# Performance work log

Measured on AMD Instinct MI355X. Metric: run time of the kernel, lower is better.

Reference implementation:

```python
import jax, jax.numpy as jnp
import numpy as np

EPS = 1e-6
ROPE_THETA = 1000000.0
SPAN_LENGTHS = [700, 300, 600, 448]
L, D, H, HK, DH, FF = 2, 2048, 16, 8, 128, 8192


def _rmsnorm(x, w):
    var = jnp.mean(jnp.square(x), axis=-1, keepdims=True)
    return x * jax.lax.rsqrt(var + EPS) * w


def _rotate_half(x):
    x1, x2 = jnp.split(x, 2, axis=-1)
    return jnp.concatenate([-x2, x1], axis=-1)


def setup_inputs() -> dict:
    key = jax.random.key(0)
    ks = jax.random.split(key, 8)
    s = 0.02  # init scale
    seg = np.repeat(np.arange(len(SPAN_LENGTHS), dtype=np.int32), SPAN_LENGTHS)
    pos = np.concatenate([np.arange(n, dtype=np.int32) for n in SPAN_LENGTHS])
    T = seg.shape[0]
    return {
        "hidden_states": jax.random.normal(ks[0], (T, D), jnp.float32),
        "ln1_w": jnp.ones((L, D), jnp.float32),
        "ln2_w": jnp.ones((L, D), jnp.float32),
        "wq": jax.random.normal(ks[1], (L, D, H * DH), jnp.float32) * s,
        "wk": jax.random.normal(ks[2], (L, D, HK * DH), jnp.float32) * s,
        "wv": jax.random.normal(ks[3], (L, D, HK * DH), jnp.float32) * s,
        "wo": jax.random.normal(ks[4], (L, H * DH, D), jnp.float32) * s,
        "qn_w": jnp.ones((L, DH), jnp.float32),
        "kn_w": jnp.ones((L, DH), jnp.float32),
        "wg": jax.random.normal(ks[5], (L, D, FF), jnp.float32) * s,
        "wu": jax.random.normal(ks[6], (L, D, FF), jnp.float32) * s,
        "wd": jax.random.normal(ks[7], (L, FF, D), jnp.float32) * s,
        "final_norm_w": jnp.ones((D,), jnp.float32),
        "segment_ids": jnp.asarray(seg),
        "position_ids": jnp.asarray(pos),
    }


def reference(hidden_states, ln1_w, ln2_w, wq, wk, wv, wo, qn_w, kn_w, wg, wu, wd, final_norm_w, segment_ids, position_ids):
    T = hidden_states.shape[0]
    # rotary tables from per-request positions (positions reset per span)
    inv_freq = 1.0 / (ROPE_THETA ** (jnp.arange(0, DH, 2, dtype=jnp.float32) / DH))
    freqs = position_ids.astype(jnp.float32)[:, None] * inv_freq  # [T, DH/2]
    emb = jnp.concatenate([freqs, freqs], axis=-1)                # [T, DH]
    cos = jnp.cos(emb)[:, None, :]
    sin = jnp.sin(emb)[:, None, :]
    # ragged causal mask: attend only within the same request span, causally
    tok = jnp.arange(T)
    mask = (segment_ids[:, None] == segment_ids[None, :]) & (tok[:, None] >= tok[None, :])
    neg = jnp.finfo(hidden_states.dtype).min
    scale = 1.0 / np.sqrt(DH)

    x = hidden_states
    for l in range(L):
        h = _rmsnorm(x, ln1_w[l])
        q = (h @ wq[l]).reshape(T, H, DH)
        k = (h @ wk[l]).reshape(T, HK, DH)
        v = (h @ wv[l]).reshape(T, HK, DH)
        q = _rmsnorm(q, qn_w[l])  # Qwen3 per-head q/k RMSNorm
        k = _rmsnorm(k, kn_w[l])
        q = q * cos + _rotate_half(q) * sin
        k = k * cos + _rotate_half(k) * sin
        rep = H // HK  # GQA
        k = jnp.repeat(k, rep, axis=1)
        v = jnp.repeat(v, rep, axis=1)
        scores = jnp.einsum('thd,shd->hts', q, k) * scale  # [H, T, T]
        scores = jnp.where(mask[None], scores, neg)
        attn = jax.nn.softmax(scores, axis=-1)
        o = jnp.einsum('hts,shd->thd', attn, v).reshape(T, H * DH)
        x = x + o @ wo[l]
        h = _rmsnorm(x, ln2_w[l])
        x = x + (jax.nn.silu(h @ wg[l]) * (h @ wu[l])) @ wd[l]
    return _rmsnorm(x, final_norm_w)
```

## Files before the change

### kernel.cpp

```cpp
#include <hip/hip_runtime.h>
#include <stdint.h>

#define T_SEQ 2048
#define DMODEL 2048
#define NH 16
#define NKV 8
#define DHEAD 128
#define DFF 8192

typedef float f32x4 __attribute__((ext_vector_type(4)));
typedef float f32x2 __attribute__((ext_vector_type(2)));
typedef __bf16 bf16x8 __attribute__((ext_vector_type(8)));
typedef unsigned short ushort8 __attribute__((ext_vector_type(8)));
typedef unsigned short ushort_t;

typedef __attribute__((address_space(1))) void gvoid;
typedef __attribute__((address_space(3))) void lvoid;

__device__ inline unsigned short f2bf(float f) {
  unsigned int u = __float_as_uint(f);
  u += 0x7fffu + ((u >> 16) & 1u);
  return (unsigned short)(u >> 16);
}
__device__ inline float bf2f(unsigned short h) {
  return __uint_as_float(((unsigned int)h) << 16);
}

__device__ inline void gload_lds16(const void* g, void* l) {
  __builtin_amdgcn_global_load_lds((gvoid*)g, (lvoid*)l, 16, 0, 0);
}

template <typename TIN>
__device__ __forceinline__ void transpose_tile(const TIN* __restrict__ in,
                                               ushort_t* __restrict__ out,
                                               int R, int C, int rmode,
                                               int bx, int by) {
  __shared__ float tile[64 * 72];
  int tid = threadIdx.x;
  int r0 = by * 64, c0 = bx * 64;
  int rl = tid >> 4;
  int cc = tid & 15;
#pragma unroll
  for (int i = 0; i < 4; ++i) {
    int row = rl + i * 16;
    const TIN* src = in + (size_t)(r0 + row) * C + c0 + cc * 4;
    float v0, v1, v2, v3;
    if constexpr (sizeof(TIN) == 4) {
      f32x4 v = *(const f32x4*)src;
      v0 = v.x; v1 = v.y; v2 = v.z; v3 = v.w;
    } else {
      ushort4 v = *(const ushort4*)src;
      v0 = bf2f(v.x); v1 = bf2f(v.y); v2 = bf2f(v.z); v3 = bf2f(v.w);
    }
    int chunk = cc ^ (row & 15);
    f32x4 t = {v0, v1, v2, v3};
    *(f32x4*)&tile[row * 72 + chunk * 4] = t;
  }
  __syncthreads();
#pragma unroll
  for (int i = 0; i < 4; ++i) {
    int nrow = rl + i * 16;
    int k4 = cc * 4;
    ushort4 o;
    {
      int k = k4 + 0;
      o.x = f2bf(tile[k * 72 + (((nrow >> 2) ^ (k & 15)) << 2) + (nrow & 3)]);
      k = k4 + 1;
      o.y = f2bf(tile[k * 72 + (((nrow >> 2) ^ (k & 15)) << 2) + (nrow & 3)]);
      k = k4 + 2;
      o.z = f2bf(tile[k * 72 + (((nrow >> 2) ^ (k & 15)) << 2) + (nrow & 3)]);
      k = k4 + 3;
      o.w = f2bf(tile[k * 72 + (((nrow >> 2) ^ (k & 15)) << 2) + (nrow & 3)]);
    }
    int n = c0 + nrow;
    int orow = n;
    if (rmode == 1) orow = ((n >> 4) << 5) + (n & 15);
    else if (rmode == 2) orow = ((n >> 4) << 5) + 16 + (n & 15);
    *(ushort4*)(out + (size_t)orow * R + r0 + k4) = o;
  }
}

template <typename TIN>
__global__ __launch_bounds__(256) void k_transpose_bf16(const TIN* __restrict__ in,
                                                        ushort_t* __restrict__ out,
                                                        int R, int C, int rmode) {
  transpose_tile<TIN>(in, out, R, C, rmode, blockIdx.x, blockIdx.y);
}

__global__ __launch_bounds__(256) void k_transpose_qkv(const float* __restrict__ wq,
                                                       const float* __restrict__ wk,
                                                       const float* __restrict__ wv,
                                                       ushort_t* __restrict__ out) {
  int z = blockIdx.z;
  const float* in;
  ushort_t* o;
  int C;
  if (z == 0) { in = wq; o = out; C = 2048; }
  else if (z == 1) { in = wk; o = out + (size_t)2048 * 2048; C = 1024; }
  else { in = wv; o = out + (size_t)3072 * 2048; C = 1024; }
  if ((int)blockIdx.x * 64 >= C) return;
  transpose_tile<float>(in, o, 2048, C, 0, blockIdx.x, blockIdx.y);
}

__global__ __launch_bounds__(256) void k_transpose_gu(const float* __restrict__ wg,
                                                      const float* __restrict__ wu,
                                                      ushort_t* __restrict__ out) {
  int z = blockIdx.z;
  transpose_tile<float>(z ? wu : wg, out, 2048, 8192, z ? 2 : 1,
                        blockIdx.x, blockIdx.y);
}

template <int BF16OUT>
__global__ __launch_bounds__(256) void k_rmsnorm(const float* __restrict__ X,
                                                 const float* __restrict__ W,
                                                 void* __restrict__ OUT) {
  int row = blockIdx.x, tid = threadIdx.x;
  const float* xr = X + (size_t)row * DMODEL;
  f32x4 x0 = *(const f32x4*)(xr + tid * 4);
  f32x4 x1 = *(const f32x4*)(xr + 1024 + tid * 4);
  float ss = x0.x * x0.x + x0.y * x0.y + x0.z * x0.z + x0.w * x0.w +
             x1.x * x1.x + x1.y * x1.y + x1.z * x1.z + x1.w * x1.w;
#pragma unroll
  for (int o = 1; o < 64; o <<= 1) ss += __shfl_xor(ss, o, 64);
  __shared__ float red[4];
  int w = tid >> 6;
  if ((tid & 63) == 0) red[w] = ss;
  __syncthreads();
  float tot = red[0] + red[1] + red[2] + red[3];
  float sc = rsqrtf(tot / (float)DMODEL + 1e-6f);
  f32x4 w0 = *(const f32x4*)(W + tid * 4);
  f32x4 w1 = *(const f32x4*)(W + 1024 + tid * 4);
  if constexpr (BF16OUT) {
    ushort_t* o = (ushort_t*)OUT + (size_t)row * DMODEL;
    ushort4 a, b;
    a.x = f2bf(x0.x * sc * w0.x); a.y = f2bf(x0.y * sc * w0.y);
    a.z = f2bf(x0.z * sc * w0.z); a.w = f2bf(x0.w * sc * w0.w);
    b.x = f2bf(x1.x * sc * w1.x); b.y = f2bf(x1.y * sc * w1.y);
    b.z = f2bf(x1.z * sc * w1.z); b.w = f2bf(x1.w * sc * w1.w);
    *(ushort4*)(o + tid * 4) = a;
    *(ushort4*)(o + 1024 + tid * 4) = b;
  } else {
    float* o = (float*)OUT + (size_t)row * DMODEL;
    f32x4 a = {x0.x * sc * w0.x, x0.y * sc * w0.y, x0.z * sc * w0.z, x0.w * sc * w0.w};
    f32x4 b = {x1.x * sc * w1.x, x1.y * sc * w1.y, x1.z * sc * w1.z, x1.w * sc * w1.w};
    *(f32x4*)(o + tid * 4) = a;
    *(f32x4*)(o + 1024 + tid * 4) = b;
  }
}

template <int NZ, int WRITEH>
__global__ __launch_bounds__(512) void k_redln(const ushort_t* __restrict__ P,
                                               const float* __restrict__ RES,
                                               const float* __restrict__ W,
                                               float* __restrict__ OUT,
                                               ushort_t* __restrict__ HB) {
  int row = blockIdx.x, tid = threadIdx.x;
  size_t base = (size_t)row * DMODEL + tid * 4;
  f32x4 v = *(const f32x4*)(RES + base);
#pragma unroll
  for (int z = 0; z < NZ; ++z) {
    ushort4 t = *(const ushort4*)(P + (size_t)z * T_SEQ * DMODEL + base);
    v.x += bf2f(t.x); v.y += bf2f(t.y); v.z += bf2f(t.z); v.w += bf2f(t.w);
  }
  if constexpr (WRITEH != 2) *(f32x4*)(OUT + base) = v;
  if constexpr (WRITEH >= 1) {
    float ss = v.x * v.x + v.y * v.y + v.z * v.z + v.w * v.w;
#pragma unroll
    for (int o = 1; o < 64; o <<= 1) ss += __shfl_xor(ss, o, 64);
    __shared__ float red[8];
    if ((tid & 63) == 0) red[tid >> 6] = ss;
    __syncthreads();
    float tot = 0.f;
#pragma unroll
    for (int i = 0; i < 8; ++i) tot += red[i];
    float sc = rsqrtf(tot / (float)DMODEL + 1e-6f);
    f32x4 wv = *(const f32x4*)(W + tid * 4);
    if constexpr (WRITEH == 1) {
      ushort4 h;
      h.x = f2bf(v.x * sc * wv.x); h.y = f2bf(v.y * sc * wv.y);
      h.z = f2bf(v.z * sc * wv.z); h.w = f2bf(v.w * sc * wv.w);
      *(ushort4*)(HB + base) = h;
    } else {
      f32x4 o = {v.x * sc * wv.x, v.y * sc * wv.y, v.z * sc * wv.z, v.w * sc * wv.w};
      *(f32x4*)(OUT + base) = o;
    }
  }
}

#define EPI_STOREB 3
#define EPI_GLU 5

#define LOADB(dst, bs, rbase)                                                  \
  {                                                                            \
    _Pragma("unroll") for (int ks = 0; ks < 2; ++ks)                           \
        _Pragma("unroll") for (int ni = 0; ni < 2; ++ni)                       \
            dst[ks][ni] = *(const bf16x8*)((bs) +                              \
                (((rbase) + ni * 16 + lr) << 6) +                              \
                ((((ks << 2) + lg) ^ (lr & 7)) << 3));                         \
  }

#define MFMA_Q(q, B)                                                           \
  {                                                                            \
    _Pragma("unroll") for (int ks = 0; ks < 2; ++ks)                           \
        _Pragma("unroll") for (int mi = 0; mi < 4; ++mi)                       \
            _Pragma("unroll") for (int ni = 0; ni < 2; ++ni)                   \
                acc[mi][(q) * 2 + ni] =                                        \
                    __builtin_amdgcn_mfma_f32_16x16x32_bf16(                   \
                        af[ks][mi], B[ks][ni], acc[mi][(q) * 2 + ni], 0, 0, 0); \
  }

template <int LAST>
__device__ __forceinline__ void g256_iter(
    const ushort_t* __restrict__ as, const ushort_t* __restrict__ bsA,
    const ushort_t* __restrict__ bsB, ushort_t* __restrict__ nA,
    ushort_t* __restrict__ nB, const ushort_t* __restrict__ an,
    const ushort_t* __restrict__ bn, size_t rs, int slds, int lr, int lg,
    f32x4 (&acc)[4][8]) {
  bf16x8 af[2][4], b0[2][2], b1[2][2];
#pragma unroll
  for (int ks = 0; ks < 2; ++ks)
#pragma unroll
    for (int mi = 0; mi < 4; ++mi)
      af[ks][mi] = *(const bf16x8*)(as + ((mi * 16 + lr) << 6) +
                                    ((((ks << 2) + lg) ^ (lr & 7)) << 3));
  LOADB(b0, bsA, 0);
  if constexpr (!LAST) {
    gload_lds16(an, nA + slds);
    gload_lds16(an + rs, nA + 4096 + slds);
    gload_lds16(an + 2 * rs, nA + 8192 + slds);
    gload_lds16(an + 3 * rs, nA + 12288 + slds);
    gload_lds16(bn, nB + slds);
    gload_lds16(bn + rs, nB + 4096 + slds);
    gload_lds16(bn + 2 * rs, nB + 8192 + slds);
    gload_lds16(bn + 3 * rs, nB + 12288 + slds);
  }
  LOADB(b1, bsA, 32);
  asm volatile("s_waitcnt lgkmcnt(4)" ::: "memory");
  __builtin_amdgcn_sched_barrier(0);
  __builtin_amdgcn_s_setprio(1);
  MFMA_Q(0, b0);
  __builtin_amdgcn_s_setprio(0);
  LOADB(b0, bsB, 0);
  asm volatile("s_waitcnt lgkmcnt(4)" ::: "memory");
  __builtin_amdgcn_sched_barrier(0);
  __builtin_amdgcn_s_setprio(1);
  MFMA_Q(1, b1);
  __builtin_amdgcn_s_setprio(0);
  LOADB(b1, bsB, 32);
  asm volatile("s_waitcnt lgkmcnt(4)" ::: "memory");
  __builtin_amdgcn_sched_barrier(0);
  __builtin_amdgcn_s_setprio(1);
  MFMA_Q(2, b0);
  __builtin_amdgcn_s_setprio(0);
  asm volatile("s_waitcnt lgkmcnt(0)" ::: "memory");
  __builtin_amdgcn_sched_barrier(0);
  __builtin_amdgcn_s_setprio(1);
  MFMA_Q(3, b1);
  __builtin_amdgcn_s_setprio(0);
  if constexpr (!LAST) {
    asm volatile("s_waitcnt vmcnt(0)" ::: "memory");
    __builtin_amdgcn_s_barrier();
  }
}

template <int EPI>
__global__ __launch_bounds__(512, 2) void k_gemm256(
    const ushort_t* __restrict__ A, const ushort_t* __restrict__ BT,
    ushort_t* __restrict__ CB, int N, int Kstride, int Kc, size_t zoff) {
  __shared__ ushort_t lds[65536];
  const int tid = threadIdx.x;
  const int l = tid & 63, wid = tid >> 6;
  const int wm = wid >> 1, wn = wid & 1;
  const int lr = l & 15, lg = l >> 4;
  const int gx = gridDim.x;
  const int nwg = gx * gridDim.y;
  const int bid = blockIdx.x + gx * blockIdx.y;
  const int chunk = nwg >> 3;
  const int x = bid & 7;
  const int local = bid >> 3;
  const int cn = chunk >> 2;
  const int ncx = gx / cn;
  const int m0 = ((x / ncx) * 4 + local / cn) * 256;
  const int n0 = ((x % ncx) * cn + local % cn) * 256;
  const int z = blockIdx.z;
  const int NT = Kc >> 6;

  A += (size_t)z * Kc;
  BT += (size_t)z * Kc;
  CB += (size_t)z * zoff;

  const int srow = tid >> 3;
  const int scs = (tid & 7) ^ (srow & 7);
  const size_t sgoff = (size_t)srow * Kstride + scs * 8;
  const int slds = wid * 512;

  const ushort_t* ga = A + (size_t)m0 * Kstride + sgoff;
  const ushort_t* gb = BT + (size_t)n0 * Kstride + sgoff;
  const size_t rs = (size_t)64 * Kstride;

  f32x4 acc[4][8] = {};

  ushort_t* Ab0 = lds;
  ushort_t* Bb0 = lds + 16384;
  ushort_t* Ab1 = lds + 32768;
  ushort_t* Bb1 = lds + 49152;

  gload_lds16(ga, Ab0 + slds);
  gload_lds16(ga + rs, Ab0 + 4096 + slds);
  gload_lds16(ga + 2 * rs, Ab0 + 8192 + slds);
  gload_lds16(ga + 3 * rs, Ab0 + 12288 + slds);
  gload_lds16(gb, Bb0 + slds);
  gload_lds16(gb + rs, Bb0 + 4096 + slds);
  gload_lds16(gb + 2 * rs, Bb0 + 8192 + slds);
  gload_lds16(gb + 3 * rs, Bb0 + 12288 + slds);
  asm volatile("s_waitcnt vmcnt(0)" ::: "memory");
  __builtin_amdgcn_s_barrier();

  for (int kt = 0; kt < NT - 1; ++kt) {
    const int d = kt & 1;
    const ushort_t* as = (d ? Ab1 : Ab0) + wm * 4096;
    const ushort_t* bsA = (d ? Bb1 : Bb0) + (wn * 2) * 4096;
    ushort_t* nA = d ? Ab0 : Ab1;
    ushort_t* nB = d ? Bb0 : Bb1;
    g256_iter<0>(as, bsA, bsA + 4096, nA, nB, ga + (size_t)(kt + 1) * 64,
                 gb + (size_t)(kt + 1) * 64, rs, slds, lr, lg, acc);
  }
  {
    const int d = (NT - 1) & 1;
    const ushort_t* as = (d ? Ab1 : Ab0) + wm * 4096;
    const ushort_t* bsA = (d ? Bb1 : Bb0) + (wn * 2) * 4096;
    g256_iter<1>(as, bsA, bsA + 4096, nullptr, nullptr, nullptr, nullptr, rs,
                 slds, lr, lg, acc);
  }

  if constexpr (EPI == EPI_GLU) {
#pragma unroll
    for (int mi = 0; mi < 4; ++mi)
#pragma unroll
      for (int ci = 0; ci < 8; ci += 2)
#pragma unroll
        for (int rr = 0; rr < 4; ++rr) {
          int m = m0 + wm * 64 + mi * 16 + lg * 4 + rr;
          int nblk = n0 + wn * 128 + ci * 16;
          int col = ((nblk >> 5) << 4) + lr;
          float gv = acc[mi][ci][rr];
          float uv = acc[mi][ci + 1][rr];
          float s = gv / (1.f + __expf(-gv));
          CB[(size_t)m * 8192 + col] = f2bf(s * uv);
        }
  } else {
#pragma unroll
    for (int mi = 0; mi < 4; ++mi)
#pragma unroll
      for (int ci = 0; ci < 8; ++ci)
#pragma unroll
        for (int rr = 0; rr < 4; ++rr) {
          int m = m0 + wm * 64 + mi * 16 + lg * 4 + rr;
          int n = n0 + wn * 128 + ci * 16 + lr;
          CB[(size_t)m * N + n] = f2bf(acc[mi][ci][rr]);
        }
  }
}

__global__ __launch_bounds__(64) void k_ropetab(const int* __restrict__ POS,
                                                float* __restrict__ CS,
                                                float* __restrict__ SN) {
  int t = blockIdx.x, d = threadIdx.x;
  const float K2 = 19.931568569324174f / 64.f;
  float ang = (float)POS[t] * exp2f(-(float)d * K2);
  CS[t * 64 + d] = cosf(ang);
  SN[t * 64 + d] = sinf(ang);
}

__global__ __launch_bounds__(256) void k_qkv_post(const ushort_t* __restrict__ Q0,
                                                  const ushort_t* __restrict__ Q1,
                                                  const float* __restrict__ QNW,
                                                  const float* __restrict__ KNW,
                                                  const float* __restrict__ CS,
                                                  const float* __restrict__ SN,
                                                  ushort_t* __restrict__ Qb,
                                                  ushort_t* __restrict__ Kb,
                                                  ushort_t* __restrict__ Vb) {
  int t = blockIdx.x, tid = threadIdx.x;
  int slot = tid >> 3, sub = tid & 7;
  int d0 = sub * 16;
  size_t off = (size_t)t * 4096 + slot * 128 + d0;
  ushort8 a0 = *(const ushort8*)(Q0 + off);
  ushort8 a1 = *(const ushort8*)(Q0 + off + 8);
  ushort8 b0 = *(const ushort8*)(Q1 + off);
  ushort8 b1 = *(const ushort8*)(Q1 + off + 8);
  float v[16];
#pragma unroll
  for (int e = 0; e < 8; ++e) {
    v[e] = bf2f(a0[e]) + bf2f(b0[e]);
    v[8 + e] = bf2f(a1[e]) + bf2f(b1[e]);
  }
  float ss = 0.f;
#pragma unroll
  for (int e = 0; e < 16; ++e) ss += v[e] * v[e];
#pragma unroll
  for (int o = 1; o < 8; o <<= 1) ss += __shfl_xor(ss, o, 64);
  ushort_t* dst;
  if (slot < 16) dst = Qb + (size_t)t * 2048 + slot * 128 + d0;
  else if (slot < 24) dst = Kb + (size_t)t * 1024 + (slot - 16) * 128 + d0;
  else dst = Vb + (size_t)t * 1024 + (slot - 24) * 128 + d0;
  ushort8 o0, o1;
  if (slot < 24) {
    float sc = rsqrtf(ss * (1.f / 128.f) + 1e-6f);
    const float* nw = (slot < 16) ? QNW : KNW;
    float w[16], cs[16], sn[16];
    int ci = t * 64 + (d0 & 63);
#pragma unroll
    for (int i = 0; i < 4; ++i) {
      *(f32x4*)&w[i * 4] = *(const f32x4*)(nw + d0 + i * 4);
      *(f32x4*)&cs[i * 4] = *(const f32x4*)(CS + ci + i * 4);
      *(f32x4*)&sn[i * 4] = *(const f32x4*)(SN + ci + i * 4);
    }
#pragma unroll
    for (int e = 0; e < 16; ++e) v[e] = v[e] * sc * w[e];
    float o[16];
#pragma unroll
    for (int e = 0; e < 16; ++e) {
      float p = __shfl_xor(v[e], 4, 64);
      float rot = (sub < 4) ? -p : p;
      o[e] = v[e] * cs[e] + rot * sn[e];
    }
#pragma unroll
    for (int e = 0; e < 8; ++e) {
      o0[e] = f2bf(o[e]);
      o1[e] = f2bf(o[8 + e]);
    }
  } else {
#pragma unroll
    for (int e = 0; e < 8; ++e) {
      o0[e] = f2bf(v[e]);
      o1[e] = f2bf(v[8 + e]);
    }
  }
  *(ushort8*)dst = o0;
  *(ushort8*)(dst + 8) = o1;
}

__global__ __launch_bounds__(64) void k_flash(const ushort_t* __restrict__ Qb,
                                              const ushort_t* __restrict__ Kb,
                                              const ushort_t* __restrict__ VT,
                                              const int* __restrict__ SEG,
                                              ushort_t* __restrict__ Ob) {
  __shared__ ushort_t Pl[2][16 * 40];
  int l = threadIdx.x;
  int qt = blockIdx.x, kvh = blockIdx.y;
  int q0 = qt * 16;
  int lr = l & 15, lg = l >> 4;
  int h0 = kvh * 2;
  bf16x8 qf0[4], qf1[4];
  {
    const bf16x8* qv = (const bf16x8*)(Qb + (size_t)(q0 + lr) * 2048 + h0 * 128);
#pragma unroll
    for (int kk = 0; kk < 4; ++kk) {
      qf0[kk] = qv[kk * 4 + lg];
      qf1[kk] = qv[16 + kk * 4 + lg];
    }
  }
  int segq[4];
#pragma unroll
  for (int r = 0; r < 4; ++r) segq[r] = SEG[q0 + lg * 4 + r];
  int target = SEG[q0];
  int lo = 0, hi = q0;
  while (lo < hi) {
    int mid = (lo + hi) >> 1;
    if (SEG[mid] < target) lo = mid + 1; else hi = mid;
  }
  int s_start = lo & ~31;
  float mr[2][4], lrun[2][4];
  f32x4 acc[2][8] = {};
#pragma unroll
  for (int h = 0; h < 2; ++h)
#pragma unroll
    for (int r = 0; r < 4; ++r) { mr[h][r] = -1e30f; lrun[h][r] = 0.f; }
  const float scale = 0.08838834764831845f;
  bf16x8 kc[8];
  {
    int sac = min(s_start + lr, T_SEQ - 1), sbc = min(s_start + 16 + lr, T_SEQ - 1);
    const bf16x8* ka = (const bf16x8*)(Kb + (size_t)sac * 1024 + kvh * 128);
    const bf16x8* kb_ = (const bf16x8*)(Kb + (size_t)sbc * 1024 + kvh * 128);
#pragma unroll
    for (int kk = 0; kk < 4; ++kk) {
      kc[kk] = ka[kk * 4 + lg];
      kc[4 + kk] = kb_[kk * 4 + lg];
    }
  }
  for (int s0 = s_start; s0 < q0 + 16; s0 += 32) {
    int sa = s0 + lr, sb = s0 + 16 + lr;
    int sac = min(sa, T_SEQ - 1), sbc = min(sb, T_SEQ - 1);
    bf16x8 vfr[8];
    int sbase = min(s0 + lg * 8, T_SEQ - 8);
#pragma unroll
    for (int c = 0; c < 8; ++c)
      vfr[c] = *(const bf16x8*)(VT + (size_t)(kvh * 128 + c * 16 + lr) * T_SEQ + sbase);
    bf16x8 kn[8];
    {
      int nsa = min(s0 + 32 + lr, T_SEQ - 1), nsb = min(s0 + 48 + lr, T_SEQ - 1);
      const bf16x8* ka = (const bf16x8*)(Kb + (size_t)nsa * 1024 + kvh * 128);
      const bf16x8* kb_ = (const bf16x8*)(Kb + (size_t)nsb * 1024 + kvh * 128);
#pragma unroll
      for (int kk = 0; kk < 4; ++kk) {
        kn[kk] = ka[kk * 4 + lg];
        kn[4 + kk] = kb_[kk * 4 + lg];
      }
    }
    f32x4 SA0 = {}, SB0 = {}, SA1 = {}, SB1 = {};
#pragma unroll
    for (int kk = 0; kk < 4; ++kk) {
      SA0 = __builtin_amdgcn_mfma_f32_16x16x32_bf16(qf0[kk], kc[kk], SA0, 0, 0, 0);
      SB0 = __builtin_amdgcn_mfma_f32_16x16x32_bf16(qf0[kk], kc[4 + kk], SB0, 0, 0, 0);
      SA1 = __builtin_amdgcn_mfma_f32_16x16x32_bf16(qf1[kk], kc[kk], SA1, 0, 0, 0);
      SB1 = __builtin_amdgcn_mfma_f32_16x16x32_bf16(qf1[kk], kc[4 + kk], SB1, 0, 0, 0);
    }
    int sga = SEG[sac], sgb = SEG[sbc];
    bool mAv[4], mBv[4];
#pragma unroll
    for (int r = 0; r < 4; ++r) {
      int qrow = q0 + lg * 4 + r;
      mAv[r] = (sa <= qrow) && (sga == segq[r]);
      mBv[r] = (sb <= qrow) && (sgb == segq[r]);
    }
#pragma unroll
    for (int h = 0; h < 2; ++h) {
#pragma unroll
      for (int r = 0; r < 4; ++r) {
        float sva = (h ? SA1[r] : SA0[r]);
        float svb = (h ? SB1[r] : SB0[r]);
        float xa = mAv[r] ? sva * scale : -1e30f;
        float xb = mBv[r] ? svb * scale : -1e30f;
        float mx = fmaxf(xa, xb);
#pragma unroll
        for (int o = 1; o < 16; o <<= 1) mx = fmaxf(mx, __shfl_xor(mx, o, 64));
        float nm = fmaxf(mr[h][r], mx);
        float ea = __expf(xa - nm), eb = __expf(xb - nm);
        float rsum = ea + eb;
#pragma unroll
        for (int o = 1; o < 16; o <<= 1) rsum += __shfl_xor(rsum, o, 64);
        float al = __expf(mr[h][r] - nm);
        lrun[h][r] = lrun[h][r] * al + rsum;
        mr[h][r] = nm;
#pragma unroll
        for (int c = 0; c < 8; ++c) acc[h][c][r] *= al;
        Pl[h][(lg * 4 + r) * 40 + lr] = f2bf(ea);
        Pl[h][(lg * 4 + r) * 40 + 16 + lr] = f2bf(eb);
      }
    }
    asm volatile("s_waitcnt lgkmcnt(0)" ::: "memory");
    bf16x8 pa0 = *(const bf16x8*)&Pl[0][lr * 40 + lg * 8];
    bf16x8 pa1 = *(const bf16x8*)&Pl[1][lr * 40 + lg * 8];
#pragma unroll
    for (int c = 0; c < 8; ++c) {
      acc[0][c] = __builtin_amdgcn_mfma_f32_16x16x32_bf16(pa0, vfr[c], acc[0][c], 0, 0, 0);
      acc[1][c] = __builtin_amdgcn_mfma_f32_16x16x32_bf16(pa1, vfr[c], acc[1][c], 0, 0, 0);
    }
#pragma unroll
    for (int j = 0; j < 8; ++j) kc[j] = kn[j];
  }
#pragma unroll
  for (int h = 0; h < 2; ++h)
#pragma unroll
    for (int c = 0; c < 8; ++c)
#pragma unroll
      for (int r = 0; r < 4; ++r) {
        float ov = acc[h][c][r] / lrun[h][r];
        Ob[(size_t)(q0 + lg * 4 + r) * 2048 + (h0 + h) * 128 + c * 16 + lr] = f2bf(ov);
      }
}

extern "C" void kernel_launch(void* const* d_in, const int* in_sizes, int n_in,
                              void* d_out, int out_size, void* d_ws, size_t ws_size,
                              hipStream_t stream) {
  const float* hidden = (const float*)d_in[0];
  const float* ln1 = (const float*)d_in[1];
  const float* ln2 = (const float*)d_in[2];
  const float* wq = (const float*)d_in[3];
  const float* wk = (const float*)d_in[4];
  const float* wv = (const float*)d_in[5];
  const float* wo = (const float*)d_in[6];
  const float* qnw = (const float*)d_in[7];
  const float* knw = (const float*)d_in[8];
  const float* wg = (const float*)d_in[9];
  const float* wu = (const float*)d_in[10];
  const float* wd = (const float*)d_in[11];
  const float* fnw = (const float*)d_in[12];
  const int* seg = (const int*)d_in[13];
  const int* pos = (const int*)d_in[14];
  float* out = (float*)d_out;

  char* ws = (char*)d_ws;
  size_t off = 0;
  auto alloc = [&](size_t bytes) {
    char* p = ws + off;
    off += (bytes + 255) & ~(size_t)255;
    return p;
  };
  ushort_t* wT = (ushort_t*)alloc((size_t)2 * DFF * DMODEL * 2);
  ushort_t* hbuf = (ushort_t*)alloc((size_t)T_SEQ * DMODEL * 2);
  ushort_t* qb = (ushort_t*)alloc((size_t)T_SEQ * 2048 * 2);
  ushort_t* kb = (ushort_t*)alloc((size_t)T_SEQ * 1024 * 2);
  ushort_t* vb = (ushort_t*)alloc((size_t)T_SEQ * 1024 * 2);
  ushort_t* vT = (ushort_t*)alloc((size_t)T_SEQ * 1024 * 2);
  ushort_t* ob = (ushort_t*)alloc((size_t)T_SEQ * 2048 * 2);
  ushort_t* qkvp = (ushort_t*)alloc((size_t)2 * T_SEQ * 4096 * 2);
  ushort_t* pbuf = (ushort_t*)alloc((size_t)4 * T_SEQ * DMODEL * 2);
  ushort_t* mbuf = (ushort_t*)alloc((size_t)T_SEQ * DFF * 2);
  float* cstab = (float*)alloc((size_t)T_SEQ * 64 * 4);
  float* sntab = (float*)alloc((size_t)T_SEQ * 64 * 4);
  (void)ws_size; (void)in_sizes; (void)n_in; (void)out_size;

  dim3 b256(256), b64(64), b512(512);
  k_ropetab<<<T_SEQ, b64, 0, stream>>>(pos, cstab, sntab);
  k_rmsnorm<1><<<T_SEQ, b256, 0, stream>>>(hidden, ln1, hbuf);

  for (int lyr = 0; lyr < 2; ++lyr) {
    const float* xsrc = (lyr == 0) ? hidden : out;

    const float* wql = wq + (size_t)lyr * DMODEL * 2048;
    const float* wkl = wk + (size_t)lyr * DMODEL * 1024;
    const float* wvl = wv + (size_t)lyr * DMODEL * 1024;
    k_transpose_qkv<<<dim3(32, 32, 3), b256, 0, stream>>>(wql, wkl, wvl, wT);
    k_gemm256<EPI_STOREB><<<dim3(16, 8, 2), b512, 0, stream>>>(
        hbuf, wT, qkvp, 4096, 2048, 1024, (size_t)2048 * 4096);
    k_qkv_post<<<T_SEQ, b256, 0, stream>>>(qkvp, qkvp + (size_t)2048 * 4096,
                                           qnw + (size_t)lyr * 128, knw + (size_t)lyr * 128,
                                           cstab, sntab, qb, kb, vb);
    k_transpose_bf16<ushort_t><<<dim3(16, 32), b256, 0, stream>>>(vb, vT, 2048, 1024, 0);
    k_flash<<<dim3(T_SEQ / 16, NKV), b64, 0, stream>>>(qb, kb, vT, seg, ob);

    const float* wol = wo + (size_t)lyr * 2048 * DMODEL;
    k_transpose_bf16<float><<<dim3(32, 32), b256, 0, stream>>>(wol, wT, 2048, 2048, 0);
    k_gemm256<EPI_STOREB><<<dim3(8, 8, 4), b512, 0, stream>>>(
        ob, wT, pbuf, 2048, 2048, 512, (size_t)2048 * 2048);
    k_redln<4, 1><<<T_SEQ, b512, 0, stream>>>(pbuf, xsrc,
                                              ln2 + (size_t)lyr * DMODEL, out, hbuf);

    const float* wgl = wg + (size_t)lyr * DMODEL * DFF;
    const float* wul = wu + (size_t)lyr * DMODEL * DFF;
    const float* wdl = wd + (size_t)lyr * DFF * DMODEL;
    k_transpose_gu<<<dim3(128, 32, 2), b256, 0, stream>>>(wgl, wul, wT);
    k_gemm256<EPI_GLU><<<dim3(64, 8, 1), b512, 0, stream>>>(
        hbuf, wT, mbuf, 16384, 2048, 2048, 0);
    k_transpose_bf16<float><<<dim3(32, 128), b256, 0, stream>>>(wdl, wT, 8192, 2048, 0);
    k_gemm256<EPI_STOREB><<<dim3(8, 8, 4), b512, 0, stream>>>(
        mbuf, wT, pbuf, 2048, 8192, 2048, (size_t)2048 * 2048);
    if (lyr == 0) {
      k_redln<4, 1><<<T_SEQ, b512, 0, stream>>>(pbuf, out, ln1 + DMODEL, out, hbuf);
    } else {
      k_redln<4, 2><<<T_SEQ, b512, 0, stream>>>(pbuf, out, fnw, out, nullptr);
    }
  }
}
```

Before: 833.6 us.

## Shrink GEMM tile to 256x128 with K-step 32 for higher occupancy

Replaces the 256x256x64 GEMM tile with a 256x128 tile and a 32-wide K step. This cuts LDS use from 128KB to 48KB and raises launch bounds to 4 blocks per CU, and every GEMM launch doubles its grid in x. The aim is better occupancy and wave-count balance across CUs. In exchange, arithmetic intensity per tile drops, barriers per unit of K double, and the previous finely interleaved LDS-load/MFMA schedule becomes a simpler two-phase one.

```diff
diff --git a/kernel.cpp b/kernel.cpp
--- a/kernel.cpp
+++ b/kernel.cpp
@@ -190,84 +190,11 @@
 #define EPI_STOREB 3
 #define EPI_GLU 5
 
-#define LOADB(dst, bs, rbase)                                                  \
-  {                                                                            \
-    _Pragma("unroll") for (int ks = 0; ks < 2; ++ks)                           \
-        _Pragma("unroll") for (int ni = 0; ni < 2; ++ni)                       \
-            dst[ks][ni] = *(const bf16x8*)((bs) +                              \
-                (((rbase) + ni * 16 + lr) << 6) +                              \
-                ((((ks << 2) + lg) ^ (lr & 7)) << 3));                         \
-  }
-
-#define MFMA_Q(q, B)                                                           \
-  {                                                                            \
-    _Pragma("unroll") for (int ks = 0; ks < 2; ++ks)                           \
-        _Pragma("unroll") for (int mi = 0; mi < 4; ++mi)                       \
-            _Pragma("unroll") for (int ni = 0; ni < 2; ++ni)                   \
-                acc[mi][(q) * 2 + ni] =                                        \
-                    __builtin_amdgcn_mfma_f32_16x16x32_bf16(                   \
-                        af[ks][mi], B[ks][ni], acc[mi][(q) * 2 + ni], 0, 0, 0); \
-  }
-
-template <int LAST>
-__device__ __forceinline__ void g256_iter(
-    const ushort_t* __restrict__ as, const ushort_t* __restrict__ bsA,
-    const ushort_t* __restrict__ bsB, ushort_t* __restrict__ nA,
-    ushort_t* __restrict__ nB, const ushort_t* __restrict__ an,
-    const ushort_t* __restrict__ bn, size_t rs, int slds, int lr, int lg,
-    f32x4 (&acc)[4][8]) {
-  bf16x8 af[2][4], b0[2][2], b1[2][2];
-#pragma unroll
-  for (int ks = 0; ks < 2; ++ks)
-#pragma unroll
-    for (int mi = 0; mi < 4; ++mi)
-      af[ks][mi] = *(const bf16x8*)(as + ((mi * 16 + lr) << 6) +
-                                    ((((ks << 2) + lg) ^ (lr & 7)) << 3));
-  LOADB(b0, bsA, 0);
-  if constexpr (!LAST) {
-    gload_lds16(an, nA + slds);
-    gload_lds16(an + rs, nA + 4096 + slds);
-    gload_lds16(an + 2 * rs, nA + 8192 + slds);
-    gload_lds16(an + 3 * rs, nA + 12288 + slds);
-    gload_lds16(bn, nB + slds);
-    gload_lds16(bn + rs, nB + 4096 + slds);
-    gload_lds16(bn + 2 * rs, nB + 8192 + slds);
-    gload_lds16(bn + 3 * rs, nB + 12288 + slds);
-  }
-  LOADB(b1, bsA, 32);
-  asm volatile("s_waitcnt lgkmcnt(4)" ::: "memory");
-  __builtin_amdgcn_sched_barrier(0);
-  __builtin_amdgcn_s_setprio(1);
-  MFMA_Q(0, b0);
-  __builtin_amdgcn_s_setprio(0);
-  LOADB(b0, bsB, 0);
-  asm volatile("s_waitcnt lgkmcnt(4)" ::: "memory");
-  __builtin_amdgcn_sched_barrier(0);
-  __builtin_amdgcn_s_setprio(1);
-  MFMA_Q(1, b1);
-  __builtin_amdgcn_s_setprio(0);
-  LOADB(b1, bsB, 32);
-  asm volatile("s_waitcnt lgkmcnt(4)" ::: "memory");
-  __builtin_amdgcn_sched_barrier(0);
-  __builtin_amdgcn_s_setprio(1);
-  MFMA_Q(2, b0);
-  __builtin_amdgcn_s_setprio(0);
-  asm volatile("s_waitcnt lgkmcnt(0)" ::: "memory");
-  __builtin_amdgcn_sched_barrier(0);
-  __builtin_amdgcn_s_setprio(1);
-  MFMA_Q(3, b1);
-  __builtin_amdgcn_s_setprio(0);
-  if constexpr (!LAST) {
-    asm volatile("s_waitcnt vmcnt(0)" ::: "memory");
-    __builtin_amdgcn_s_barrier();
-  }
-}
-
 template <int EPI>
-__global__ __launch_bounds__(512, 2) void k_gemm256(
+__global__ __launch_bounds__(512, 4) void k_gemm256(
     const ushort_t* __restrict__ A, const ushort_t* __restrict__ BT,
     ushort_t* __restrict__ CB, int N, int Kstride, int Kc, size_t zoff) {
-  __shared__ ushort_t lds[65536];
+  __shared__ ushort_t lds[24576];
   const int tid = threadIdx.x;
   const int l = tid & 63, wid = tid >> 6;
   const int wm = wid >> 1, wn = wid & 1;
@@ -281,67 +208,90 @@
   const int cn = chunk >> 2;
   const int ncx = gx / cn;
   const int m0 = ((x / ncx) * 4 + local / cn) * 256;
-  const int n0 = ((x % ncx) * cn + local % cn) * 256;
+  const int n0 = ((x % ncx) * cn + local % cn) * 128;
   const int z = blockIdx.z;
-  const int NT = Kc >> 6;
+  const int NT = Kc >> 5;
 
   A += (size_t)z * Kc;
   BT += (size_t)z * Kc;
   CB += (size_t)z * zoff;
 
-  const int srow = tid >> 3;
-  const int scs = (tid & 7) ^ (srow & 7);
-  const size_t sgoff = (size_t)srow * Kstride + scs * 8;
-  const int slds = wid * 512;
+  const int sr = tid >> 2;
+  const int sc = (tid & 3) ^ ((tid >> 3) & 3);
+  const size_t sgoff = (size_t)sr * Kstride + sc * 8;
+  const size_t rs128 = (size_t)128 * Kstride;
+  const int sldsw = wid * 512;
 
   const ushort_t* ga = A + (size_t)m0 * Kstride + sgoff;
   const ushort_t* gb = BT + (size_t)n0 * Kstride + sgoff;
-  const size_t rs = (size_t)64 * Kstride;
-
-  f32x4 acc[4][8] = {};
+
+  f32x4 acc[4][4] = {};
 
   ushort_t* Ab0 = lds;
-  ushort_t* Bb0 = lds + 16384;
-  ushort_t* Ab1 = lds + 32768;
-  ushort_t* Bb1 = lds + 49152;
-
-  gload_lds16(ga, Ab0 + slds);
-  gload_lds16(ga + rs, Ab0 + 4096 + slds);
-  gload_lds16(ga + 2 * rs, Ab0 + 8192 + slds);
-  gload_lds16(ga + 3 * rs, Ab0 + 12288 + slds);
-  gload_lds16(gb, Bb0 + slds);
-  gload_lds16(gb + rs, Bb0 + 4096 + slds);
-  gload_lds16(gb + 2 * rs, Bb0 + 8192 + slds);
-  gload_lds16(gb + 3 * rs, Bb0 + 12288 + slds);
+  ushort_t* Bb0 = lds + 8192;
+  ushort_t* Ab1 = lds + 12288;
+  ushort_t* Bb1 = lds + 20480;
+
+  gload_lds16(ga, Ab0 + sldsw);
+  gload_lds16(ga + rs128, Ab0 + 4096 + sldsw);
+  gload_lds16(gb, Bb0 + sldsw);
   asm volatile("s_waitcnt vmcnt(0)" ::: "memory");
   __builtin_amdgcn_s_barrier();
 
-  for (int kt = 0; kt < NT - 1; ++kt) {
+  const int sw = (lg ^ ((lr >> 1) & 3)) * 8;
+  for (int kt = 0; kt < NT; ++kt) {
     const int d = kt & 1;
-    const ushort_t* as = (d ? Ab1 : Ab0) + wm * 4096;
-    const ushort_t* bsA = (d ? Bb1 : Bb0) + (wn * 2) * 4096;
+    const ushort_t* as = (d ? Ab1 : Ab0) + (wm * 64) * 32;
+    const ushort_t* bs = (d ? Bb1 : Bb0) + (wn * 64) * 32;
     ushort_t* nA = d ? Ab0 : Ab1;
     ushort_t* nB = d ? Bb0 : Bb1;
-    g256_iter<0>(as, bsA, bsA + 4096, nA, nB, ga + (size_t)(kt + 1) * 64,
-                 gb + (size_t)(kt + 1) * 64, rs, slds, lr, lg, acc);
-  }
-  {
-    const int d = (NT - 1) & 1;
-    const ushort_t* as = (d ? Ab1 : Ab0) + wm * 4096;
-    const ushort_t* bsA = (d ? Bb1 : Bb0) + (wn * 2) * 4096;
-    g256_iter<1>(as, bsA, bsA + 4096, nullptr, nullptr, nullptr, nullptr, rs,
-                 slds, lr, lg, acc);
+    const ushort_t* an = ga + (size_t)(kt + 1) * 32;
+    const ushort_t* bn = gb + (size_t)(kt + 1) * 32;
+    bf16x8 af[4], bfr[4];
+#pragma unroll
+    for (int mi = 0; mi < 4; ++mi)
+      af[mi] = *(const bf16x8*)(as + (mi * 16 + lr) * 32 + sw);
+#pragma unroll
+    for (int ci = 0; ci < 4; ++ci)
+      bfr[ci] = *(const bf16x8*)(bs + (ci * 16 + lr) * 32 + sw);
+    if (kt + 1 < NT) {
+      gload_lds16(an, nA + sldsw);
+      gload_lds16(an + rs128, nA + 4096 + sldsw);
+      gload_lds16(bn, nB + sldsw);
+    }
+    asm volatile("s_waitcnt lgkmcnt(2)" ::: "memory");
+    __builtin_amdgcn_sched_barrier(0);
+    __builtin_amdgcn_s_setprio(1);
+#pragma unroll
+    for (int mi = 0; mi < 4; ++mi) {
+      acc[mi][0] = __builtin_amdgcn_mfma_f32_16x16x32_bf16(af[mi], bfr[0], acc[mi][0], 0, 0, 0);
+      acc[mi][1] = __builtin_amdgcn_mfma_f32_16x16x32_bf16(af[mi], bfr[1], acc[mi][1], 0, 0, 0);
+    }
+    __builtin_amdgcn_s_setprio(0);
+    asm volatile("s_waitcnt lgkmcnt(0)" ::: "memory");
+    __builtin_amdgcn_sched_barrier(0);
+    __builtin_amdgcn_s_setprio(1);
+#pragma unroll
+    for (int mi = 0; mi < 4; ++mi) {
+      acc[mi][2] = __builtin_amdgcn_mfma_f32_16x16x32_bf16(af[mi], bfr[2], acc[mi][2], 0, 0, 0);
+      acc[mi][3] = __builtin_amdgcn_mfma_f32_16x16x32_bf16(af[mi], bfr[3], acc[mi][3], 0, 0, 0);
+    }
+    __builtin_amdgcn_s_setprio(0);
+    if (kt + 1 < NT) {
+      asm volatile("s_waitcnt vmcnt(0)" ::: "memory");
+      __builtin_amdgcn_s_barrier();
+    }
   }
 
   if constexpr (EPI == EPI_GLU) {
 #pragma unroll
     for (int mi = 0; mi < 4; ++mi)
 #pragma unroll
-      for (int ci = 0; ci < 8; ci += 2)
+      for (int ci = 0; ci < 4; ci += 2)
 #pragma unroll
         for (int rr = 0; rr < 4; ++rr) {
           int m = m0 + wm * 64 + mi * 16 + lg * 4 + rr;
-          int nblk = n0 + wn * 128 + ci * 16;
+          int nblk = n0 + wn * 64 + ci * 16;
           int col = ((nblk >> 5) << 4) + lr;
           float gv = acc[mi][ci][rr];
           float uv = acc[mi][ci + 1][rr];
@@ -352,11 +302,11 @@
 #pragma unroll
     for (int mi = 0; mi < 4; ++mi)
 #pragma unroll
-      for (int ci = 0; ci < 8; ++ci)
+      for (int ci = 0; ci < 4; ++ci)
 #pragma unroll
         for (int rr = 0; rr < 4; ++rr) {
           int m = m0 + wm * 64 + mi * 16 + lg * 4 + rr;
-          int n = n0 + wn * 128 + ci * 16 + lr;
+          int n = n0 + wn * 64 + ci * 16 + lr;
           CB[(size_t)m * N + n] = f2bf(acc[mi][ci][rr]);
         }
   }
@@ -623,7 +573,7 @@
     const float* wkl = wk + (size_t)lyr * DMODEL * 1024;
     const float* wvl = wv + (size_t)lyr * DMODEL * 1024;
     k_transpose_qkv<<<dim3(32, 32, 3), b256, 0, stream>>>(wql, wkl, wvl, wT);
-    k_gemm256<EPI_STOREB><<<dim3(16, 8, 2), b512, 0, stream>>>(
+    k_gemm256<EPI_STOREB><<<dim3(32, 8, 2), b512, 0, stream>>>(
         hbuf, wT, qkvp, 4096, 2048, 1024, (size_t)2048 * 4096);
     k_qkv_post<<<T_SEQ, b256, 0, stream>>>(qkvp, qkvp + (size_t)2048 * 4096,
                                            qnw + (size_t)lyr * 128, knw + (size_t)lyr * 128,
@@ -633,7 +583,7 @@
 
     const float* wol = wo + (size_t)lyr * 2048 * DMODEL;
     k_transpose_bf16<float><<<dim3(32, 32), b256, 0, stream>>>(wol, wT, 2048, 2048, 0);
-    k_gemm256<EPI_STOREB><<<dim3(8, 8, 4), b512, 0, stream>>>(
+    k_gemm256<EPI_STOREB><<<dim3(16, 8, 4), b512, 0, stream>>>(
         ob, wT, pbuf, 2048, 2048, 512, (size_t)2048 * 2048);
     k_redln<4, 1><<<T_SEQ, b512, 0, stream>>>(pbuf, xsrc,
                                               ln2 + (size_t)lyr * DMODEL, out, hbuf);
@@ -642,10 +592,10 @@
     const float* wul = wu + (size_t)lyr * DMODEL * DFF;
     const float* wdl = wd + (size_t)lyr * DFF * DMODEL;
     k_transpose_gu<<<dim3(128, 32, 2), b256, 0, stream>>>(wgl, wul, wT);
-    k_gemm256<EPI_GLU><<<dim3(64, 8, 1), b512, 0, stream>>>(
+    k_gemm256<EPI_GLU><<<dim3(128, 8, 1), b512, 0, stream>>>(
         hbuf, wT, mbuf, 16384, 2048, 2048, 0);
     k_transpose_bf16<float><<<dim3(32, 128), b256, 0, stream>>>(wdl, wT, 8192, 2048, 0);
-    k_gemm256<EPI_STOREB><<<dim3(8, 8, 4), b512, 0, stream>>>(
+    k_gemm256<EPI_STOREB><<<dim3(16, 8, 4), b512, 0, stream>>>(
         mbuf, wT, pbuf, 2048, 8192, 2048, (size_t)2048 * 2048);
     if (lyr == 0) {
       k_redln<4, 1><<<T_SEQ, b512, 0, stream>>>(pbuf, out, ln1 + DMODEL, out, hbuf);
```

Result: slower. 902.8 us (+8.3%).
